# Optimization experiments

Hardware: AMD Instinct MI355X
Metric: run time of the kernel (lower is better)

Reference implementation:

```python
import jax, jax.numpy as jnp
import numpy as np


def _gcn_conv(x, src, dst, W, b, n_nodes):
    # PyG GCNConv: add self-loops, symmetric normalization D^-1/2 A D^-1/2,
    # linear transform, scatter-add aggregation, bias.
    loop = jnp.arange(n_nodes, dtype=src.dtype)
    s = jnp.concatenate([src, loop])
    d = jnp.concatenate([dst, loop])
    deg = jax.ops.segment_sum(jnp.ones_like(s, dtype=x.dtype), d, num_segments=n_nodes)
    dinv = jnp.where(deg > 0, jax.lax.rsqrt(deg), 0.0)
    norm = dinv[s] * dinv[d]                      # [E+N]
    h = x @ W                                     # [N, H] dense GEMM
    msg = h[s] * norm[:, None]                    # [E+N, H] gathered messages
    out = jax.ops.segment_sum(msg, d, num_segments=n_nodes)  # scatter-add
    return out + b


def setup_inputs() -> dict:
    key = jax.random.key(0)
    ks = jax.random.split(key, 8)
    n_nodes, n_edges, d_in, hidden, num_graphs = 10000, 160000, 512, 512, 64
    x = jax.random.normal(ks[0], (n_nodes, d_in), dtype=jnp.float32)
    edge_index = jax.random.randint(ks[1], (2, n_edges), 0, n_nodes, dtype=jnp.int64)
    batch = jnp.sort(jax.random.randint(ks[2], (n_nodes,), 0, num_graphs, dtype=jnp.int64))
    # Xavier-uniform-ish weights (GCNConv lin has no bias separate in newer PyG; keep W+b per layer)
    def xavier(k, shape):
        fan_in, fan_out = shape[0], shape[1]
        lim = np.sqrt(6.0 / (fan_in + fan_out))
        return jax.random.uniform(k, shape, jnp.float32, -lim, lim)
    W1 = xavier(ks[3], (d_in, hidden))
    b1 = jnp.zeros((hidden,), jnp.float32)
    W2 = xavier(ks[4], (hidden, hidden))
    b2 = jnp.zeros((hidden,), jnp.float32)
    Wlin = xavier(ks[5], (hidden, 1))
    blin = jnp.zeros((1,), jnp.float32)
    return {"x": x, "edge_index": edge_index, "batch": batch, "num_graphs": num_graphs,
            "W1": W1, "b1": b1, "W2": W2, "b2": b2, "Wlin": Wlin, "blin": blin}


def reference(x, edge_index, batch, num_graphs, W1, b1, W2, b2, Wlin, blin):
    n_nodes = x.shape[0]
    src, dst = edge_index[0], edge_index[1]
    h = _gcn_conv(x, src, dst, W1, b1, n_nodes)
    h = jax.nn.relu(h)
    h = _gcn_conv(h, src, dst, W2, b2, n_nodes)
    pooled = jax.ops.segment_sum(h, batch, num_segments=num_graphs)  # global_add_pool
    return pooled @ Wlin + blin  # [num_graphs, 1]
```

## Files before the change

### kernel.cpp

```cpp
#include <hip/hip_runtime.h>
#include <stdint.h>

typedef __attribute__((ext_vector_type(8))) short s16x8;
typedef __attribute__((ext_vector_type(8))) unsigned short u16x8;
typedef __attribute__((ext_vector_type(4))) float f32x4;

#define D 512
#define BM 128
#define BK 64
#define CAP 96

__device__ __forceinline__ unsigned short f2bf(float f) {
    unsigned u = __float_as_uint(f);
    return (unsigned short)((u + 0x7FFFu + ((u >> 16) & 1u)) >> 16);
}
__device__ __forceinline__ float bf2f(unsigned short h) {
    return __uint_as_float(((unsigned)h) << 16);
}

__global__ __launch_bounds__(256) void k_prep(const float* W1, const float* W2,
                                              const float* Wlin, const float* b2,
                                              const float* blin, int* fill, float* z,
                                              unsigned short* w1t, float* w2l, float* out,
                                              int nN, int nG) {
    int b = blockIdx.x, t = threadIdx.x;
    if (b < 64) {
        __shared__ float tile[64][65];
        int ti = b >> 3, tj = b & 7;
#pragma unroll
        for (int p = 0; p < 4; ++p) {
            int r = p * 16 + (t >> 4);
            int c = (t & 15) * 4;
            float4 v = *(const float4*)(W1 + (size_t)(ti * 64 + r) * D + tj * 64 + c);
            tile[r][c] = v.x; tile[r][c + 1] = v.y; tile[r][c + 2] = v.z; tile[r][c + 3] = v.w;
        }
        __syncthreads();
        int c = t >> 2;
        int r0 = (t & 3) * 16;
        u16x8 o0, o1;
#pragma unroll
        for (int i = 0; i < 8; ++i) o0[i] = f2bf(tile[r0 + i][c]);
#pragma unroll
        for (int i = 0; i < 8; ++i) o1[i] = f2bf(tile[r0 + 8 + i][c]);
        unsigned short* wp = w1t + (size_t)(tj * 64 + c) * D + ti * 64 + r0;
        *(u16x8*)wp = o0;
        *(u16x8*)(wp + 8) = o1;
    } else if (b < 104) {
        int i = (b - 64) * 256 + t;
        if (i < nN) { fill[i] = 0; z[i] = 0.f; }
    } else if (b < 233) {
        int i = (b - 104) * 4 + (t >> 6);
        int l = t & 63;
        if (i < D + 1) {
            const float* row = (i < D) ? (W2 + (size_t)i * D) : b2;
            float4 a0 = *(const float4*)(row + l * 8);
            float4 a1 = *(const float4*)(row + l * 8 + 4);
            float4 c0 = *(const float4*)(Wlin + l * 8);
            float4 c1 = *(const float4*)(Wlin + l * 8 + 4);
            float p = a0.x * c0.x + a0.y * c0.y + a0.z * c0.z + a0.w * c0.w
                    + a1.x * c1.x + a1.y * c1.y + a1.z * c1.z + a1.w * c1.w;
#pragma unroll
            for (int o = 32; o > 0; o >>= 1) p += __shfl_xor(p, o);
            if (l == 0) w2l[i] = p;
        }
    } else {
        if (t < nG) out[t] = blin[0];
    }
}

__global__ __launch_bounds__(256) void k_gemm_scatter(const float* X, const unsigned short* BT,
                                                      unsigned short* C, int Mreal,
                                                      const int* src, const int* dst,
                                                      int* fill, int* csr_src, int nE) {
    __shared__ unsigned short As[BM * BK];
    __shared__ unsigned short Bs[BM * BK];
    int b = blockIdx.x;
    if (b >= 316) {
        int e = (b - 316) * 256 + threadIdx.x;
        if (e < nE) {
            int s = src[e], d = dst[e];
            int pos = atomicAdd(&fill[d], 1);
            if (pos < CAP) csr_src[(size_t)d * CAP + pos] = s;
        }
        return;
    }
    int tn0 = (b & 3) * BM, tm0 = (b >> 2) * BM;
    int t = threadIdx.x, lane = t & 63, wave = t >> 6;
    int wr = wave >> 1, wc = wave & 1;
    f32x4 acc[4][4] = {};
    int r15 = lane & 15;
    int khalf = lane >> 4;

    for (int k0 = 0; k0 < D; k0 += BK) {
        __syncthreads();
        {
            int rb0 = wave * 8;
#pragma unroll
            for (int c = 0; c < 4; ++c) {
                int rbase = c * 32 + rb0;
                int row = rbase + (lane >> 3);
                int kg = (lane & 7) ^ (row & 7);
                const unsigned short* gsrc = BT + (size_t)(tn0 + row) * D + k0 + kg * 8;
                __builtin_amdgcn_global_load_lds(
                    (const __attribute__((address_space(1))) unsigned int*)gsrc,
                    (__attribute__((address_space(3))) unsigned int*)(Bs + rbase * BK),
                    16, 0, 0);
            }
        }
#pragma unroll
        for (int i = 0; i < 4; ++i) {
            int idx = t + 256 * i;
            int row = idx >> 3, kg = idx & 7;
            int grow = tm0 + row; if (grow >= Mreal) grow = Mreal - 1;
            const float* gp = X + (size_t)grow * D + k0 + kg * 8;
            float4 f0 = *(const float4*)gp;
            float4 f1 = *(const float4*)(gp + 4);
            u16x8 o;
            o[0] = f2bf(f0.x); o[1] = f2bf(f0.y); o[2] = f2bf(f0.z); o[3] = f2bf(f0.w);
            o[4] = f2bf(f1.x); o[5] = f2bf(f1.y); o[6] = f2bf(f1.z); o[7] = f2bf(f1.w);
            *(u16x8*)&As[row * BK + (kg ^ (row & 7)) * 8] = o;
        }
        __syncthreads();
#pragma unroll
        for (int ks = 0; ks < 2; ++ks) {
            int g = ks * 4 + khalf;
            s16x8 a[4], bb[4];
#pragma unroll
            for (int m = 0; m < 4; ++m) {
                int row = wr * 64 + m * 16 + r15;
                a[m] = *(const s16x8*)&As[row * BK + (g ^ (row & 7)) * 8];
            }
#pragma unroll
            for (int n = 0; n < 4; ++n) {
                int row = wc * 64 + n * 16 + r15;
                bb[n] = *(const s16x8*)&Bs[row * BK + (g ^ (row & 7)) * 8];
            }
#pragma unroll
            for (int m = 0; m < 4; ++m)
#pragma unroll
                for (int n = 0; n < 4; ++n)
                    acc[m][n] = __builtin_amdgcn_mfma_f32_16x16x32_bf16(a[m], bb[n], acc[m][n], 0, 0, 0);
        }
    }

    int cr = (lane >> 4) * 4;
    int cc = lane & 15;
#pragma unroll
    for (int m = 0; m < 4; ++m)
#pragma unroll
        for (int n = 0; n < 4; ++n)
#pragma unroll
            for (int r = 0; r < 4; ++r) {
                int row = tm0 + wr * 64 + m * 16 + cr + r;
                if (row < Mreal) {
                    int col = tn0 + wc * 64 + n * 16 + cc;
                    C[(size_t)row * D + col] = f2bf(acc[m][n][r]);
                }
            }
}

__global__ __launch_bounds__(256) void k_agg1(const unsigned short* h1b, const int* csr_src,
                                              const int* fill, const float* b1,
                                              const float* w2l, float* z, int nN) {
    int bid = blockIdx.x;
    int xcd = bid & 7;
    int slice = xcd >> 1;
    int chunk = (bid >> 3) * 2 + (xcd & 1);
    int t = threadIdx.x;
    int g = t >> 4;
    int l = t & 15;
    int v = chunk * 16 + g;
    if (v >= nN) return;
    int f0 = (slice << 7) + l * 8;

    float acc[8];
    float4 ba = *(const float4*)(b1 + f0);
    float4 bb = *(const float4*)(b1 + f0 + 4);
    acc[0] = ba.x; acc[1] = ba.y; acc[2] = ba.z; acc[3] = ba.w;
    acc[4] = bb.x; acc[5] = bb.y; acc[6] = bb.z; acc[7] = bb.w;

    int deg = fill[v];
    float degv1 = (float)(deg + 1);
    float wself = 1.0f / degv1;
    u16x8 hv = *(const u16x8*)(h1b + (size_t)v * D + f0);
#pragma unroll
    for (int j = 0; j < 8; ++j) acc[j] += wself * bf2f(hv[j]);

    const int* row = csr_src + (size_t)v * CAP;
    int sb = (g & 3) << 4;
    for (int eb = 0; eb < deg; eb += 16) {
        int n = deg - eb; if (n > 16) n = 16;
        int myi = 0; float myw = 0.f;
        if (l < n) {
            myi = row[eb + l];
            myw = rsqrtf((float)(fill[myi] + 1) * degv1);
        }
        int j = 0;
        for (; j + 4 <= n; j += 4) {
            int s0 = __shfl(myi, sb + j),     s1 = __shfl(myi, sb + j + 1);
            int s2 = __shfl(myi, sb + j + 2), s3 = __shfl(myi, sb + j + 3);
            float w0 = __shfl(myw, sb + j),     w1 = __shfl(myw, sb + j + 1);
            float w2 = __shfl(myw, sb + j + 2), w3 = __shfl(myw, sb + j + 3);
            u16x8 h0 = *(const u16x8*)(h1b + (size_t)s0 * D + f0);
            u16x8 h1 = *(const u16x8*)(h1b + (size_t)s1 * D + f0);
            u16x8 h2 = *(const u16x8*)(h1b + (size_t)s2 * D + f0);
            u16x8 h3 = *(const u16x8*)(h1b + (size_t)s3 * D + f0);
#pragma unroll
            for (int q = 0; q < 8; ++q) acc[q] += w0 * bf2f(h0[q]);
#pragma unroll
            for (int q = 0; q < 8; ++q) acc[q] += w1 * bf2f(h1[q]);
#pragma unroll
            for (int q = 0; q < 8; ++q) acc[q] += w2 * bf2f(h2[q]);
#pragma unroll
            for (int q = 0; q < 8; ++q) acc[q] += w3 * bf2f(h3[q]);
        }
        for (; j < n; ++j) {
            int s = __shfl(myi, sb + j);
            float w = __shfl(myw, sb + j);
            u16x8 hs = *(const u16x8*)(h1b + (size_t)s * D + f0);
#pragma unroll
            for (int q = 0; q < 8; ++q) acc[q] += w * bf2f(hs[q]);
        }
    }

    float4 wa = *(const float4*)(w2l + f0);
    float4 wb = *(const float4*)(w2l + f0 + 4);
    float wv[8] = {wa.x, wa.y, wa.z, wa.w, wb.x, wb.y, wb.z, wb.w};
    float p = 0.f;
#pragma unroll
    for (int j = 0; j < 8; ++j) p += fmaxf(acc[j], 0.f) * wv[j];
    p += __shfl_xor(p, 8);
    p += __shfl_xor(p, 4);
    p += __shfl_xor(p, 2);
    p += __shfl_xor(p, 1);
    if (l == 0) atomicAdd(&z[v], p);
}

__global__ __launch_bounds__(256) void k_agg2(const float* z, const int* src, const int* dst,
                                              const int* fill, const float* w2l,
                                              const int* batch, float* out, int nN, int nE, int nG) {
    __shared__ float bins[64];
    int t = threadIdx.x;
    if (t < 64) bins[t] = 0.f;
    __syncthreads();
    int i = blockIdx.x * 256 + t;
    if (i < nE) {
        int s = src[i], d = dst[i];
        float val = rsqrtf((float)(fill[s] + 1) * (float)(fill[d] + 1)) * z[s];
        int g = batch[d];
        if (g < 64) atomicAdd(&bins[g], val); else atomicAdd(&out[g], val);
    }
    if (i < nN) {
        float val = w2l[D] + z[i] / (float)(fill[i] + 1);
        int g = batch[i];
        if (g < 64) atomicAdd(&bins[g], val); else atomicAdd(&out[g], val);
    }
    __syncthreads();
    if (t < 64 && t < nG) {
        float v = bins[t];
        if (v != 0.f) atomicAdd(&out[t], v);
    }
}

extern "C" void kernel_launch(void* const* d_in, const int* in_sizes, int n_in,
                              void* d_out, int out_size, void* d_ws, size_t ws_size,
                              hipStream_t stream) {
    const float* x    = (const float*)d_in[0];
    const int*   ei   = (const int*)d_in[1];
    const int*   batch= (const int*)d_in[2];
    const float* W1   = (const float*)d_in[4];
    const float* b1   = (const float*)d_in[5];
    const float* W2   = (const float*)d_in[6];
    const float* b2   = (const float*)d_in[7];
    const float* Wlin = (const float*)d_in[8];
    const float* blin = (const float*)d_in[9];
    float* out = (float*)d_out;

    int nN = in_sizes[0] / D;
    int nE = in_sizes[1] / 2;
    int nG = out_size;
    const int* src = ei;
    const int* dst = ei + nE;
    int Mpad = (nN + BM - 1) / BM * BM;

    char* p = (char*)d_ws;
    auto alloc = [&](size_t b) { char* r = p; p += (b + 255) & ~(size_t)255; return (void*)r; };
    int*   fill    = (int*)alloc((size_t)nN * 4);
    int*   csr_src = (int*)alloc((size_t)nN * CAP * 4);
    float* z       = (float*)alloc((size_t)nN * 4);
    float* w2l     = (float*)alloc((size_t)(D + 1) * 4);
    unsigned short* w1t = (unsigned short*)alloc((size_t)D * D * 2);
    unsigned short* h1b = (unsigned short*)alloc((size_t)nN * D * 2);

    k_prep<<<234, 256, 0, stream>>>(W1, W2, Wlin, b2, blin, fill, z, w1t, w2l, out, nN, nG);
    int nb = 316 + (nE + 255) / 256;
    k_gemm_scatter<<<nb, 256, 0, stream>>>(x, w1t, h1b, nN, src, dst, fill, csr_src, nE);
    k_agg1<<<313 * 8, 256, 0, stream>>>(h1b, csr_src, fill, b1, w2l, z, nN);
    nb = (nE + 255) / 256;
    k_agg2<<<nb, 256, 0, stream>>>(z, src, dst, fill, w2l, batch, out, nN, nE, nG);
}
```

Before: 69.82 us.

## Move W2·Wlin prep into gemm launch and use one wave per node in agg1

New measurement: 79.04 us. +13.2%, slower.

```diff
diff --git a/kernel.cpp b/kernel.cpp
--- a/kernel.cpp
+++ b/kernel.cpp
@@ -18,11 +18,8 @@
     return __uint_as_float(((unsigned)h) << 16);
 }
 
-__global__ __launch_bounds__(256) void k_prep(const float* W1, const float* W2,
-                                              const float* Wlin, const float* b2,
-                                              const float* blin, int* fill, float* z,
-                                              unsigned short* w1t, float* w2l, float* out,
-                                              int nN, int nG) {
+__global__ __launch_bounds__(256) void k_prep(const float* W1, int* fill, float* z,
+                                              unsigned short* w1t, int nN) {
     int b = blockIdx.x, t = threadIdx.x;
     if (b < 64) {
         __shared__ float tile[64][65];
@@ -45,47 +42,54 @@
         unsigned short* wp = w1t + (size_t)(tj * 64 + c) * D + ti * 64 + r0;
         *(u16x8*)wp = o0;
         *(u16x8*)(wp + 8) = o1;
-    } else if (b < 104) {
+    } else {
         int i = (b - 64) * 256 + t;
         if (i < nN) { fill[i] = 0; z[i] = 0.f; }
-    } else if (b < 233) {
-        int i = (b - 104) * 4 + (t >> 6);
-        int l = t & 63;
-        if (i < D + 1) {
-            const float* row = (i < D) ? (W2 + (size_t)i * D) : b2;
-            float4 a0 = *(const float4*)(row + l * 8);
-            float4 a1 = *(const float4*)(row + l * 8 + 4);
-            float4 c0 = *(const float4*)(Wlin + l * 8);
-            float4 c1 = *(const float4*)(Wlin + l * 8 + 4);
-            float p = a0.x * c0.x + a0.y * c0.y + a0.z * c0.z + a0.w * c0.w
-                    + a1.x * c1.x + a1.y * c1.y + a1.z * c1.z + a1.w * c1.w;
-#pragma unroll
-            for (int o = 32; o > 0; o >>= 1) p += __shfl_xor(p, o);
-            if (l == 0) w2l[i] = p;
-        }
-    } else {
-        if (t < nG) out[t] = blin[0];
     }
 }
 
 __global__ __launch_bounds__(256) void k_gemm_scatter(const float* X, const unsigned short* BT,
                                                       unsigned short* C, int Mreal,
                                                       const int* src, const int* dst,
-                                                      int* fill, int* csr_src, int nE) {
+                                                      int* fill, int* csr_src, int nE,
+                                                      const float* W2, const float* Wlin,
+                                                      const float* b2, const float* blin,
+                                                      float* w2l, float* out, int nG) {
     __shared__ unsigned short As[BM * BK];
     __shared__ unsigned short Bs[BM * BK];
     int b = blockIdx.x;
+    int t = threadIdx.x;
     if (b >= 316) {
-        int e = (b - 316) * 256 + threadIdx.x;
-        if (e < nE) {
-            int s = src[e], d = dst[e];
-            int pos = atomicAdd(&fill[d], 1);
-            if (pos < CAP) csr_src[(size_t)d * CAP + pos] = s;
+        int br = b - 316;
+        if (br < 625) {
+            int e = br * 256 + t;
+            if (e < nE) {
+                int s = src[e], d = dst[e];
+                int pos = atomicAdd(&fill[d], 1);
+                if (pos < CAP) csr_src[(size_t)d * CAP + pos] = s;
+            }
+        } else if (br < 754) {
+            int i = (br - 625) * 4 + (t >> 6);
+            int l = t & 63;
+            if (i < D + 1) {
+                const float* row = (i < D) ? (W2 + (size_t)i * D) : b2;
+                float4 a0 = *(const float4*)(row + l * 8);
+                float4 a1 = *(const float4*)(row + l * 8 + 4);
+                float4 c0 = *(const float4*)(Wlin + l * 8);
+                float4 c1 = *(const float4*)(Wlin + l * 8 + 4);
+                float p = a0.x * c0.x + a0.y * c0.y + a0.z * c0.z + a0.w * c0.w
+                        + a1.x * c1.x + a1.y * c1.y + a1.z * c1.z + a1.w * c1.w;
+#pragma unroll
+                for (int o = 32; o > 0; o >>= 1) p += __shfl_xor(p, o);
+                if (l == 0) w2l[i] = p;
+            }
+        } else {
+            if (t < nG) out[t] = blin[0];
         }
         return;
     }
     int tn0 = (b & 3) * BM, tm0 = (b >> 2) * BM;
-    int t = threadIdx.x, lane = t & 63, wave = t >> 6;
+    int lane = t & 63, wave = t >> 6;
     int wr = wave >> 1, wc = wave & 1;
     f32x4 acc[4][4] = {};
     int r15 = lane & 15;
@@ -165,62 +169,55 @@
     int bid = blockIdx.x;
     int xcd = bid & 7;
     int slice = xcd >> 1;
-    int chunk = (bid >> 3) * 2 + (xcd & 1);
-    int t = threadIdx.x;
-    int g = t >> 4;
-    int l = t & 15;
-    int v = chunk * 16 + g;
+    int quad = (bid >> 3) * 2 + (xcd & 1);
+    int wave = threadIdx.x >> 6, l = threadIdx.x & 63;
+    int v = quad * 4 + wave;
     if (v >= nN) return;
-    int f0 = (slice << 7) + l * 8;
-
-    float acc[8];
-    float4 ba = *(const float4*)(b1 + f0);
-    float4 bb = *(const float4*)(b1 + f0 + 4);
-    acc[0] = ba.x; acc[1] = ba.y; acc[2] = ba.z; acc[3] = ba.w;
-    acc[4] = bb.x; acc[5] = bb.y; acc[6] = bb.z; acc[7] = bb.w;
-
+    int q = l >> 4;
+    int r = l & 15;
+    int f0 = (slice << 7) + r * 8;
+
+    float acc[8] = {0.f, 0.f, 0.f, 0.f, 0.f, 0.f, 0.f, 0.f};
     int deg = fill[v];
     float degv1 = (float)(deg + 1);
-    float wself = 1.0f / degv1;
-    u16x8 hv = *(const u16x8*)(h1b + (size_t)v * D + f0);
-#pragma unroll
-    for (int j = 0; j < 8; ++j) acc[j] += wself * bf2f(hv[j]);
+
+    if (q == 0) {
+        float4 ba = *(const float4*)(b1 + f0);
+        float4 bb = *(const float4*)(b1 + f0 + 4);
+        float wself = 1.0f / degv1;
+        u16x8 hv = *(const u16x8*)(h1b + (size_t)v * D + f0);
+        acc[0] = ba.x + wself * bf2f(hv[0]); acc[1] = ba.y + wself * bf2f(hv[1]);
+        acc[2] = ba.z + wself * bf2f(hv[2]); acc[3] = ba.w + wself * bf2f(hv[3]);
+        acc[4] = bb.x + wself * bf2f(hv[4]); acc[5] = bb.y + wself * bf2f(hv[5]);
+        acc[6] = bb.z + wself * bf2f(hv[6]); acc[7] = bb.w + wself * bf2f(hv[7]);
+    }
 
     const int* row = csr_src + (size_t)v * CAP;
-    int sb = (g & 3) << 4;
-    for (int eb = 0; eb < deg; eb += 16) {
-        int n = deg - eb; if (n > 16) n = 16;
+    for (int eb = 0; eb < deg; eb += 64) {
+        int n = deg - eb; if (n > 64) n = 64;
         int myi = 0; float myw = 0.f;
         if (l < n) {
             myi = row[eb + l];
             myw = rsqrtf((float)(fill[myi] + 1) * degv1);
         }
-        int j = 0;
-        for (; j + 4 <= n; j += 4) {
-            int s0 = __shfl(myi, sb + j),     s1 = __shfl(myi, sb + j + 1);
-            int s2 = __shfl(myi, sb + j + 2), s3 = __shfl(myi, sb + j + 3);
-            float w0 = __shfl(myw, sb + j),     w1 = __shfl(myw, sb + j + 1);
-            float w2 = __shfl(myw, sb + j + 2), w3 = __shfl(myw, sb + j + 3);
-            u16x8 h0 = *(const u16x8*)(h1b + (size_t)s0 * D + f0);
-            u16x8 h1 = *(const u16x8*)(h1b + (size_t)s1 * D + f0);
-            u16x8 h2 = *(const u16x8*)(h1b + (size_t)s2 * D + f0);
-            u16x8 h3 = *(const u16x8*)(h1b + (size_t)s3 * D + f0);
-#pragma unroll
-            for (int q = 0; q < 8; ++q) acc[q] += w0 * bf2f(h0[q]);
-#pragma unroll
-            for (int q = 0; q < 8; ++q) acc[q] += w1 * bf2f(h1[q]);
-#pragma unroll
-            for (int q = 0; q < 8; ++q) acc[q] += w2 * bf2f(h2[q]);
-#pragma unroll
-            for (int q = 0; q < 8; ++q) acc[q] += w3 * bf2f(h3[q]);
-        }
-        for (; j < n; ++j) {
-            int s = __shfl(myi, sb + j);
-            float w = __shfl(myw, sb + j);
-            u16x8 hs = *(const u16x8*)(h1b + (size_t)s * D + f0);
-#pragma unroll
-            for (int q = 0; q < 8; ++q) acc[q] += w * bf2f(hs[q]);
-        }
+#pragma unroll 2
+        for (int j = 0; j < n; j += 4) {
+            int e = j + q;
+            int ee = e < n ? e : 0;
+            int s = __shfl(myi, ee);
+            float w = __shfl(myw, ee);
+            if (e < n) {
+                u16x8 hs = *(const u16x8*)(h1b + (size_t)s * D + f0);
+#pragma unroll
+                for (int p = 0; p < 8; ++p) acc[p] += w * bf2f(hs[p]);
+            }
+        }
+    }
+
+#pragma unroll
+    for (int p = 0; p < 8; ++p) {
+        acc[p] += __shfl_xor(acc[p], 16);
+        acc[p] += __shfl_xor(acc[p], 32);
     }
 
     float4 wa = *(const float4*)(w2l + f0);
@@ -281,7 +278,6 @@
     int nG = out_size;
     const int* src = ei;
     const int* dst = ei + nE;
-    int Mpad = (nN + BM - 1) / BM * BM;
 
     char* p = (char*)d_ws;
     auto alloc = [&](size_t b) { char* r = p; p += (b + 255) & ~(size_t)255; return (void*)r; };
@@ -292,10 +288,11 @@
     unsigned short* w1t = (unsigned short*)alloc((size_t)D * D * 2);
     unsigned short* h1b = (unsigned short*)alloc((size_t)nN * D * 2);
 
-    k_prep<<<234, 256, 0, stream>>>(W1, W2, Wlin, b2, blin, fill, z, w1t, w2l, out, nN, nG);
-    int nb = 316 + (nE + 255) / 256;
-    k_gemm_scatter<<<nb, 256, 0, stream>>>(x, w1t, h1b, nN, src, dst, fill, csr_src, nE);
-    k_agg1<<<313 * 8, 256, 0, stream>>>(h1b, csr_src, fill, b1, w2l, z, nN);
+    k_prep<<<104, 256, 0, stream>>>(W1, fill, z, w1t, nN);
+    int nb = 316 + (nE + 255) / 256 + 129 + 1;
+    k_gemm_scatter<<<nb, 256, 0, stream>>>(x, w1t, h1b, nN, src, dst, fill, csr_src, nE,
+                                           W2, Wlin, b2, blin, w2l, out, nG);
+    k_agg1<<<1250 * 8, 256, 0, stream>>>(h1b, csr_src, fill, b1, w2l, z, nN);
     nb = (nE + 255) / 256;
     k_agg2<<<nb, 256, 0, stream>>>(z, src, dst, fill, w2l, batch, out, nN, nE, nG);
 }
```
